# Kernel tuning notes

Hardware: AMD Instinct MI355X
Metric: run time of the kernel (lower is better)

Reference implementation:

```python
import jax, jax.numpy as jnp
import numpy as np

G = 32            # group_dim
N = 2             # feature batch (becomes 3N after repeat)
H = 192
W = 192
C_EXTRA = 32      # channels of the extra input tensor
POOLING_SIZE = (5, 9, 17)
POOLING_CHAN = (1, 1, 1)  # scaled by group_dim inside the module


def conv1x1(x, w, b):
    # x: [B, Cin, H, W], w: [Cout, Cin], b: [Cout]
    return jnp.einsum('bchw,oc->bohw', x, w) + b[None, :, None, None]


def integral_image(x):
    # x: [B, C, H, W] -> summed-area table [B, C, H+1, W+1] with zero top row / left col
    s = jnp.cumsum(jnp.cumsum(x, axis=2), axis=3)
    return jnp.pad(s, ((0, 0), (0, 0), (1, 0), (1, 0)))


def box_sums(S, half, h, w):
    # S: [B, C, h+1, w+1]; returns per-pixel box sums [B, C, h, w] and area [h, w]
    y = jnp.arange(h)
    x = jnp.arange(w)
    y0 = jnp.maximum(y - half, 0)
    y1 = jnp.minimum(y + 1 + half, h)
    x0 = jnp.maximum(x - half, 0)
    x1 = jnp.minimum(x + 1 + half, w)
    Sy0 = S[:, :, y0, :]
    Sy1 = S[:, :, y1, :]
    s = Sy1[:, :, :, x1] - Sy1[:, :, :, x0] - Sy0[:, :, :, x1] + Sy0[:, :, :, x0]
    area = ((y1 - y0)[:, None] * (x1 - x0)[None, :]).astype(S.dtype)
    return s, area


def setup_inputs() -> dict:
    key = jax.random.key(0)
    ks = jax.random.split(key, 10)
    C = G + C_EXTRA  # channels after concat with image_ctx
    c1_out = (G + 2) // 2 * 4
    inp = {
        'feature': jax.random.normal(ks[0], (N, G, H, W), jnp.float32),
        'extra': jax.random.normal(ks[1], (3 * N, C_EXTRA, H, W), jnp.float32),
        'w_ctx': jax.random.normal(ks[2], (G, G), jnp.float32) * 0.05,
        'b_ctx': jnp.zeros((G,), jnp.float32),
        'w1': jax.random.normal(ks[3], (c1_out, C), jnp.float32) * 0.05,
        'b1': jnp.zeros((c1_out,), jnp.float32),
    }
    for i in range(3):
        oc = 2 * G * POOLING_CHAN[i]
        inp['w_s%d' % i] = jax.random.normal(ks[4 + i], (oc, 2 * C), jnp.float32) * 0.05
        inp['b_s%d' % i] = jnp.zeros((oc,), jnp.float32)
    return inp


def reference(feature, extra, w_ctx, b_ctx, w1, b1,
              w_s0, b_s0, w_s1, b_s1, w_s2, b_s2):
    img_ctx = conv1x1(feature, w_ctx, b_ctx)          # [N, G, H, W]
    img_ctx = jnp.repeat(img_ctx, 3, axis=0)          # [3N, G, H, W]
    x = jnp.concatenate([img_ctx, extra], axis=1)     # [3N, C, H, W]
    _, _, h, w = x.shape

    outs = [conv1x1(x, w1, b1)]

    S1 = integral_image(x)
    S2 = integral_image(x * x)

    scale_params = ((w_s0, b_s0), (w_s1, b_s1), (w_s2, b_s2))
    for ps, (ws, bs) in zip(POOLING_SIZE, scale_params):
        half = ps // 2
        s1, area = box_sums(S1, half, h, w)
        s2, _ = box_sums(S2, half, h, w)
        mean = s1 / area
        var = s2 / area - mean * mean
        outs.append(conv1x1(jnp.concatenate([mean, var], axis=1), ws, bs))

    return jnp.concatenate(outs, axis=1)  # [3N, 68 + 3*64 = 260, H, W]
```

## Files before the change

### kernel.cpp

```cpp
#include <hip/hip_runtime.h>

#define H 192
#define W 192
#define HW (H*W)
#define G 32
#define C 64
#define C2 128
#define C1 68
#define B 6
#define NB 2
#define OUTC 260
#define STRIP 48


__global__ __launch_bounds__(256) void ctx_kernel(
    const float* __restrict__ feature, const float* __restrict__ w_ctx,
    const float* __restrict__ b_ctx, float* __restrict__ ctx)
{
    int p = blockIdx.x * 256 + threadIdx.x;
    int b = blockIdx.y;
    float f[G];
    const float* fp = feature + (size_t)b * G * HW + p;
#pragma unroll
    for (int k = 0; k < G; k++) f[k] = fp[k * HW];
    float* op = ctx + (size_t)b * G * HW + p;
    for (int o = 0; o < G; o++) {
        float acc = b_ctx[o];
#pragma unroll
        for (int k = 0; k < G; k++) acc += w_ctx[o * G + k] * f[k];
        op[o * HW] = acc;
    }
}

__global__ __launch_bounds__(256) void conv1_kernel(
    const float* __restrict__ ctx, const float* __restrict__ extra,
    const float* __restrict__ w1, const float* __restrict__ b1,
    float* __restrict__ out)
{
    int p = blockIdx.x * 256 + threadIdx.x;
    int b = blockIdx.y;
    float xv[C];
    const float* cp = ctx + (size_t)(b / 3) * G * HW + p;
#pragma unroll
    for (int k = 0; k < G; k++) xv[k] = cp[k * HW];
    const float* ep = extra + (size_t)b * G * HW + p;
#pragma unroll
    for (int k = 0; k < G; k++) xv[G + k] = ep[k * HW];
    float* op = out + (size_t)b * OUTC * HW + p;
    for (int o = 0; o < C1; o++) {
        float acc = b1[o];
#pragma unroll
        for (int k = 0; k < C; k++) acc += w1[o * C + k] * xv[k];
        op[o * HW] = acc;
    }
}


template<int CTRL, int RM>
__device__ __forceinline__ float dpp_mov0(float x) {
    return __int_as_float(__builtin_amdgcn_update_dpp(
        0, __float_as_int(x), CTRL, RM, 0xf, false));
}
__device__ __forceinline__ float wave_iscan(float x) {
    x += dpp_mov0<0x111, 0xf>(x);
    x += dpp_mov0<0x112, 0xf>(x);
    x += dpp_mov0<0x114, 0xf>(x);
    x += dpp_mov0<0x118, 0xf>(x);
    x += dpp_mov0<0x142, 0xa>(x);
    x += dpp_mov0<0x143, 0xc>(x);
    return x;
}

__global__ __launch_bounds__(256) void transpose_wi_kernel(
    const float* __restrict__ w0, const float* __restrict__ w1,
    const float* __restrict__ w2, float* __restrict__ wTi)
{
    int i = blockIdx.x * 256 + threadIdx.x;
    if (i >= 3 * C * C2) return;
    int si = i / (C * C2);
    int r = i % (C * C2);
    const float* ws = (si == 0) ? w0 : (si == 1) ? w1 : w2;
    int o = r / C2, ci = r % C2;
    int dst = (ci < C) ? (ci * (2 * C) + o) : ((ci - C) * (2 * C) + C + o);
    wTi[si * (C2 * C) + dst] = ws[r];
}

__global__ __launch_bounds__(64) void mv_all_kernel2(
    const float* __restrict__ ctx, const float* __restrict__ extra,
    int bbase, int nbs, float* __restrict__ mv)
{
    const int hk0 = 2, hk1 = 4, hk2 = 8;
    const int hks[3] = {hk0, hk1, hk2};

    int lane = threadIdx.x;
    int c = blockIdx.x;
    int sy = blockIdx.y & 3;
    int sx = blockIdx.y >> 2;
    int bz = blockIdx.z;
    int b = bbase + bz;
    const float* src = (c < G) ? (ctx + ((size_t)(b / 3) * G + c) * HW)
                               : (extra + ((size_t)b * G + (c - G)) * HW);
    int col = sx * 48 - 8 + lane;
    bool colok = (col >= 0 && col < W);
    int h0 = sy * 48;

    float s1[3] = {0.f, 0.f, 0.f}, s2[3] = {0.f, 0.f, 0.f};
#pragma unroll
    for (int dy = -hk2; dy <= hk2; ++dy) {
        int y = h0 + dy;
        float v = (colok && y >= 0 && y < H) ? src[y * W + col] : 0.f;
        float vv = v * v;
        if (dy >= -hk0 && dy <= hk0) { s1[0] += v; s2[0] += vv; }
        if (dy >= -hk1 && dy <= hk1) { s1[1] += v; s2[1] += vv; }
        s1[2] += v; s2[2] += vv;
    }

    bool outok = (lane >= 8 && lane < 56);
    float inv_nc[3];
#pragma unroll
    for (int k = 0; k < 3; ++k) {
        int x0 = max(col - hks[k], 0), x1 = min(col + hks[k], W - 1);
        inv_nc[k] = 1.0f / (float)(x1 - x0 + 1);
    }
    size_t sstride = (size_t)nbs * C * HW;
    float2* mvp = (float2*)mv + ((size_t)bz * C + c) * HW;

    for (int h = h0; h < h0 + 48; ++h) {
        if (h > h0) {
#pragma unroll
            for (int k = 0; k < 3; ++k) {
                int ya = h + hks[k], ys = h - hks[k] - 1;
                if (colok) {
                    if (ya < H)  { float v = src[ya * W + col]; s1[k] += v; s2[k] = fmaf(v, v, s2[k]); }
                    if (ys >= 0) { float v = src[ys * W + col]; s1[k] -= v; s2[k] = fmaf(-v, v, s2[k]); }
                }
            }
        }
#pragma unroll
        for (int k = 0; k < 3; ++k) {
            float p1 = wave_iscan(s1[k]);
            float p2 = wave_iscan(s2[k]);
            int ihi = lane + hks[k];
            int ilo = lane - hks[k] - 1;
            float h1 = __shfl(p1, ihi & 63);
            float h2 = __shfl(p2, ihi & 63);
            float l1 = __shfl(p1, ilo & 63);
            float l2 = __shfl(p2, ilo & 63);
            if (ilo < 0) { l1 = 0.f; l2 = 0.f; }
            if (outok) {
                float t1 = h1 - l1;
                float t2 = h2 - l2;
                float inv_nr;
                if (h >= hks[k] && h + hks[k] < H) inv_nr = 1.0f / (float)(2 * hks[k] + 1);
                else inv_nr = 1.0f / (float)(min(h + hks[k], H - 1) - max(h - hks[k], 0) + 1);
                float ia = inv_nr * inv_nc[k];
                float mean = t1 * ia;
                float var = fmaf(t2, ia, -(mean * mean));
                mvp[(size_t)k * sstride + h * W + col] = make_float2(mean, var);
            }
        }
    }
}

__global__ __launch_bounds__(256) void sconv_all_kernel3(
    const float* __restrict__ mv, const float* __restrict__ wTi,
    const float* __restrict__ bs0, const float* __restrict__ bs1,
    const float* __restrict__ bs2,
    int bbase, int nbs, float* __restrict__ out)
{
    __shared__ float ls_w[C * 32];
    int t = threadIdx.x;
    int si = blockIdx.z >> 2;
    int og = blockIdx.z & 3;
    int bz = blockIdx.y;
    int p0 = blockIdx.x * 1024;

    const float* wp = wTi + si * (C2 * C);
#pragma unroll
    for (int i = t; i < C * 32; i += 256) {
        int c = i >> 5, j = i & 31;
        int col = (j < 16) ? (og * 16 + j) : (64 + og * 16 + (j - 16));
        ls_w[i] = wp[c * (2 * C) + col];
    }
    __syncthreads();

    size_t sstride = (size_t)nbs * C * HW;
    const float2* xbase = (const float2*)mv + (size_t)si * sstride
                        + (size_t)bz * C * HW + p0 + 4 * t;

    float acc[4][16];
#pragma unroll
    for (int px = 0; px < 4; ++px)
#pragma unroll
        for (int o = 0; o < 16; ++o) acc[px][o] = 0.f;

#pragma unroll 2
    for (int c = 0; c < C; ++c) {
        const float4* q = (const float4*)(xbase + (size_t)c * HW);
        float4 xA = q[0];
        float4 xB = q[1];
        const float4* wq = (const float4*)(ls_w + c * 32);
        float wm[16], wv[16];
        *(float4*)&wm[0]  = wq[0]; *(float4*)&wm[4]  = wq[1];
        *(float4*)&wm[8]  = wq[2]; *(float4*)&wm[12] = wq[3];
        *(float4*)&wv[0]  = wq[4]; *(float4*)&wv[4]  = wq[5];
        *(float4*)&wv[8]  = wq[6]; *(float4*)&wv[12] = wq[7];
        float m[4] = {xA.x, xA.z, xB.x, xB.z};
        float v[4] = {xA.y, xA.w, xB.y, xB.w};
#pragma unroll
        for (int px = 0; px < 4; ++px)
#pragma unroll
            for (int o = 0; o < 16; ++o)
                acc[px][o] = fmaf(wm[o], m[px], fmaf(wv[o], v[px], acc[px][o]));
    }

    const float* bs = (si == 0) ? bs0 : (si == 1) ? bs1 : bs2;
    float* op = out + ((size_t)(bbase + bz) * OUTC + C1 + si * C + og * 16) * HW
              + p0 + 4 * t;
#pragma unroll
    for (int o = 0; o < 16; ++o) {
        float bb = bs[og * 16 + o];
        float4 st = make_float4(acc[0][o] + bb, acc[1][o] + bb,
                                acc[2][o] + bb, acc[3][o] + bb);
        *(float4*)(op + (size_t)o * HW) = st;
    }
}


__global__ __launch_bounds__(256) void transpose_w_kernel(
    const float* __restrict__ wsrc, float* __restrict__ wT, int oc, int ic)
{
    int i = blockIdx.x * 256 + threadIdx.x;
    if (i >= oc * ic) return;
    int o = i / ic, c = i % ic;
    wT[c * oc + o] = wsrc[i];
}

__global__ __launch_bounds__(192) void mv_kernel(
    const float* __restrict__ ctx, const float* __restrict__ extra,
    int half, int bbase, float* __restrict__ mv)
{
    __shared__ float ls1[2][W];
    __shared__ float ls2[2][W];
    int w = threadIdx.x;
    int c = blockIdx.x;
    int s = blockIdx.y;
    int bz = blockIdx.z;
    int b = bbase + bz;
    const float* src = (c < G)
        ? (ctx + ((size_t)(b / 3) * G + c) * HW)
        : (extra + ((size_t)b * G + (c - G)) * HW);

    int h0 = s * STRIP;
    int ya = max(h0 - half, 0);
    int yb = min(h0 + half, H - 1);
    float s1 = 0.f, s2 = 0.f;
    for (int y = ya; y <= yb; y++) { float v = src[y * W + w]; s1 += v; s2 += v * v; }

    int x0 = max(w - half, 0);
    int x1 = min(w + half, W - 1);
    float ncols = (float)(x1 - x0 + 1);

    size_t obase = ((size_t)bz * C2 + c) * HW;

    for (int h = h0; h < h0 + STRIP; h++) {
        if (h > h0) {
            int yadd = h + half;
            int ysub = h - half - 1;
            if (yadd <= H - 1) { float v = src[yadd * W + w]; s1 += v; s2 += v * v; }
            if (ysub >= 0)     { float v = src[ysub * W + w]; s1 -= v; s2 -= v * v; }
        }
        int buf = h & 1;
        ls1[buf][w] = s1;
        ls2[buf][w] = s2;
        __syncthreads();
        float t1 = 0.f, t2 = 0.f;
        for (int x = x0; x <= x1; x++) { t1 += ls1[buf][x]; t2 += ls2[buf][x]; }
        int nrows = min(h + half, H - 1) - max(h - half, 0) + 1;
        float inv_area = 1.0f / ((float)nrows * ncols);
        float mean = t1 * inv_area;
        float var  = t2 * inv_area - mean * mean;
        mv[obase + h * W + w] = mean;
        mv[obase + (size_t)C * HW + h * W + w] = var;
    }
}

__global__ __launch_bounds__(256) void sconv_kernel(
    const float* __restrict__ mv, const float* __restrict__ wT,
    const float* __restrict__ bsc, int bbase, int co, float* __restrict__ out)
{
    int p = blockIdx.x * 256 + threadIdx.x;
    int bz = blockIdx.y;
    int b = bbase + bz;
    const float* xp = mv + (size_t)bz * C2 * HW + p;
    float acc[C];
#pragma unroll
    for (int o = 0; o < C; o++) acc[o] = 0.f;
#pragma unroll 2
    for (int c = 0; c < C2; c++) {
        float v = xp[(size_t)c * HW];
        const float* wrow = wT + c * C;
#pragma unroll
        for (int o = 0; o < C; o++) acc[o] += wrow[o] * v;
    }
    float* op = out + ((size_t)b * OUTC + co) * HW + p;
#pragma unroll
    for (int o = 0; o < C; o++) op[o * HW] = acc[o] + bsc[o];
}


extern "C" void kernel_launch(void* const* d_in, const int* in_sizes, int n_in,
                              void* d_out, int out_size, void* d_ws, size_t ws_size,
                              hipStream_t stream) {
    const float* feature = (const float*)d_in[0];
    const float* extra   = (const float*)d_in[1];
    const float* w_ctx   = (const float*)d_in[2];
    const float* b_ctx   = (const float*)d_in[3];
    const float* w1      = (const float*)d_in[4];
    const float* b1      = (const float*)d_in[5];
    const float* w_s[3]  = {(const float*)d_in[6], (const float*)d_in[8], (const float*)d_in[10]};
    const float* b_s[3]  = {(const float*)d_in[7], (const float*)d_in[9], (const float*)d_in[11]};
    float* out = (float*)d_out;

    float* ctx = (float*)d_ws;
    float* wT  = ctx + (size_t)NB * G * HW;
    float* mv  = wT + 3 * C2 * C;

    size_t base_bytes = ((size_t)NB * G * HW + 3 * C2 * C) * 4;
    size_t mv_new = (size_t)B * 3 * C * HW * 2 * 4;
    size_t mv_full = (size_t)B * C2 * HW * 4;
    bool newpath = ws_size >= base_bytes + mv_new;

    ctx_kernel<<<dim3(HW / 256, NB), 256, 0, stream>>>(feature, w_ctx, b_ctx, ctx);
    conv1_kernel<<<dim3(HW / 256, B), 256, 0, stream>>>(ctx, extra, w1, b1, out);

    if (newpath) {
        transpose_wi_kernel<<<dim3((3 * C * C2 + 255) / 256), 256, 0, stream>>>(
            w_s[0], w_s[1], w_s[2], wT);
        mv_all_kernel2<<<dim3(C, 16, B), 64, 0, stream>>>(ctx, extra, 0, B, mv);
        sconv_all_kernel3<<<dim3(HW / 1024, B, 12), 256, 0, stream>>>(
            mv, wT, b_s[0], b_s[1], b_s[2], 0, B, out);
    } else {
        for (int si = 0; si < 3; si++) {
            transpose_w_kernel<<<dim3((C2 * C + 255) / 256), 256, 0, stream>>>(
                w_s[si], wT + si * C2 * C, C, C2);
        }
        const int halves[3] = {2, 4, 8};
        bool batched = ws_size >= base_bytes + mv_full;
        if (batched) {
            for (int si = 0; si < 3; si++) {
                mv_kernel<<<dim3(C, H / STRIP, B), W, 0, stream>>>(ctx, extra, halves[si], 0, mv);
                sconv_kernel<<<dim3(HW / 256, B), 256, 0, stream>>>(
                    mv, wT + si * C2 * C, b_s[si], 0, C1 + si * C, out);
            }
        } else {
            for (int si = 0; si < 3; si++) {
                for (int b = 0; b < B; b++) {
                    mv_kernel<<<dim3(C, H / STRIP, 1), W, 0, stream>>>(ctx, extra, halves[si], b, mv);
                    sconv_kernel<<<dim3(HW / 256, 1), 256, 0, stream>>>(
                        mv, wT + si * C2 * C, b_s[si], b, C1 + si * C, out);
                }
            }
        }
    }
}
```

Baseline: 697.0 us.

## Retile scale conv so each block covers all output groups of one scale

The scale 1x1-conv kernel now assigns the four 16-channel output groups to the four wavefronts of one block, with each thread covering 8 pixels instead of 4. The full 128x64 weight slice sits in shared memory. Each mean/var input is then read from global memory once per scale rather than once per output group, which cuts redundant input traffic. In exchange the accumulator array doubles to 128 floats per thread, shared memory grows to 32KB, and launch bounds now request 2 blocks per SIMD, so register pressure and possible spills are the main risk.

```diff
diff --git a/kernel.cpp b/kernel.cpp
--- a/kernel.cpp
+++ b/kernel.cpp
@@ -162,67 +162,63 @@
     }
 }
 
-__global__ __launch_bounds__(256) void sconv_all_kernel3(
+__global__ __launch_bounds__(256, 2) void sconv_all_kernel4(
     const float* __restrict__ mv, const float* __restrict__ wTi,
     const float* __restrict__ bs0, const float* __restrict__ bs1,
     const float* __restrict__ bs2,
     int bbase, int nbs, float* __restrict__ out)
 {
-    __shared__ float ls_w[C * 32];
+    __shared__ float ls_w[C2 * C];
     int t = threadIdx.x;
-    int si = blockIdx.z >> 2;
-    int og = blockIdx.z & 3;
+    int pxg = t & 63;
+    int og = t >> 6;
     int bz = blockIdx.y;
-    int p0 = blockIdx.x * 1024;
+    int si = blockIdx.z;
+    int p0 = blockIdx.x * 512 + pxg * 8;
 
     const float* wp = wTi + si * (C2 * C);
-#pragma unroll
-    for (int i = t; i < C * 32; i += 256) {
-        int c = i >> 5, j = i & 31;
-        int col = (j < 16) ? (og * 16 + j) : (64 + og * 16 + (j - 16));
-        ls_w[i] = wp[c * (2 * C) + col];
-    }
+    for (int i = t; i < C2 * C; i += 256) ls_w[i] = wp[i];
     __syncthreads();
 
     size_t sstride = (size_t)nbs * C * HW;
-    const float2* xbase = (const float2*)mv + (size_t)si * sstride
-                        + (size_t)bz * C * HW + p0 + 4 * t;
-
-    float acc[4][16];
-#pragma unroll
-    for (int px = 0; px < 4; ++px)
+    const float2* xb = (const float2*)mv + (size_t)si * sstride
+                     + (size_t)bz * C * HW + p0;
+
+    float acc[8][16];
+#pragma unroll
+    for (int px = 0; px < 8; ++px)
 #pragma unroll
         for (int o = 0; o < 16; ++o) acc[px][o] = 0.f;
 
-#pragma unroll 2
     for (int c = 0; c < C; ++c) {
-        const float4* q = (const float4*)(xbase + (size_t)c * HW);
-        float4 xA = q[0];
-        float4 xB = q[1];
-        const float4* wq = (const float4*)(ls_w + c * 32);
-        float wm[16], wv[16];
-        *(float4*)&wm[0]  = wq[0]; *(float4*)&wm[4]  = wq[1];
-        *(float4*)&wm[8]  = wq[2]; *(float4*)&wm[12] = wq[3];
-        *(float4*)&wv[0]  = wq[4]; *(float4*)&wv[4]  = wq[5];
-        *(float4*)&wv[8]  = wq[6]; *(float4*)&wv[12] = wq[7];
-        float m[4] = {xA.x, xA.z, xB.x, xB.z};
-        float v[4] = {xA.y, xA.w, xB.y, xB.w};
-#pragma unroll
-        for (int px = 0; px < 4; ++px)
+        const float4* q = (const float4*)(xb + (size_t)c * HW);
+        float4 q0 = q[0], q1 = q[1], q2 = q[2], q3 = q[3];
+        float m_[8] = {q0.x, q0.z, q1.x, q1.z, q2.x, q2.z, q3.x, q3.z};
+        float v_[8] = {q0.y, q0.w, q1.y, q1.w, q2.y, q2.w, q3.y, q3.w};
+        const float4* wqm = (const float4*)(ls_w + c * C2 + og * 16);
+        const float4* wqv = (const float4*)(ls_w + c * C2 + C + og * 16);
+        float wm_[16], wv_[16];
+        *(float4*)&wm_[0]  = wqm[0]; *(float4*)&wm_[4]  = wqm[1];
+        *(float4*)&wm_[8]  = wqm[2]; *(float4*)&wm_[12] = wqm[3];
+        *(float4*)&wv_[0]  = wqv[0]; *(float4*)&wv_[4]  = wqv[1];
+        *(float4*)&wv_[8]  = wqv[2]; *(float4*)&wv_[12] = wqv[3];
+#pragma unroll
+        for (int px = 0; px < 8; ++px)
 #pragma unroll
             for (int o = 0; o < 16; ++o)
-                acc[px][o] = fmaf(wm[o], m[px], fmaf(wv[o], v[px], acc[px][o]));
+                acc[px][o] = fmaf(wm_[o], m_[px],
+                             fmaf(wv_[o], v_[px], acc[px][o]));
     }
 
     const float* bs = (si == 0) ? bs0 : (si == 1) ? bs1 : bs2;
-    float* op = out + ((size_t)(bbase + bz) * OUTC + C1 + si * C + og * 16) * HW
-              + p0 + 4 * t;
+    float* op = out + ((size_t)(bbase + bz) * OUTC + C1 + si * C + og * 16) * HW + p0;
 #pragma unroll
     for (int o = 0; o < 16; ++o) {
         float bb = bs[og * 16 + o];
-        float4 st = make_float4(acc[0][o] + bb, acc[1][o] + bb,
-                                acc[2][o] + bb, acc[3][o] + bb);
-        *(float4*)(op + (size_t)o * HW) = st;
+        *(float4*)(op + (size_t)o * HW) = make_float4(
+            acc[0][o] + bb, acc[1][o] + bb, acc[2][o] + bb, acc[3][o] + bb);
+        *(float4*)(op + (size_t)o * HW + 4) = make_float4(
+            acc[4][o] + bb, acc[5][o] + bb, acc[6][o] + bb, acc[7][o] + bb);
     }
 }
 
@@ -338,7 +334,7 @@
         transpose_wi_kernel<<<dim3((3 * C * C2 + 255) / 256), 256, 0, stream>>>(
             w_s[0], w_s[1], w_s[2], wT);
         mv_all_kernel2<<<dim3(C, 16, B), 64, 0, stream>>>(ctx, extra, 0, B, mv);
-        sconv_all_kernel3<<<dim3(HW / 1024, B, 12), 256, 0, stream>>>(
+        sconv_all_kernel4<<<dim3(HW / 512, B, 3), 256, 0, stream>>>(
             mv, wT, b_s[0], b_s[1], b_s[2], 0, B, out);
     } else {
         for (int si = 0; si < 3; si++) {
```

After: 728.1 us. +4.5%, slower.
